# Performance work log

Hardware: AMD Instinct MI355X
Metric: run time of the kernel (lower is better)

The kernel has to match this reference:

```python
import jax, jax.numpy as jnp
import numpy as np
from jax import lax

B, C, H, W = 16, 1, 1024, 1024
BOUNDARY_WEIGHT = 3.0
# two iterations of a flat 5x5 structuring element == one flat 9x9 window
WIN = 9
PAD = WIN // 2


def setup_inputs() -> dict:
    key = jax.random.key(0)
    k1, k2, k3, k4 = jax.random.split(key, 4)
    logits = jax.random.normal(k1, (B, C, H, W), dtype=jnp.float32)
    # spatially-coherent binary masks (random disks), mimicking car masks
    cy = jax.random.uniform(k2, (B,), minval=0.3 * H, maxval=0.7 * H)
    cx = jax.random.uniform(k3, (B,), minval=0.3 * W, maxval=0.7 * W)
    r = jax.random.uniform(k4, (B,), minval=0.15 * H, maxval=0.4 * H)
    ys = jnp.arange(H, dtype=jnp.float32)
    xs = jnp.arange(W, dtype=jnp.float32)
    d2 = (ys[None, :, None] - cy[:, None, None]) ** 2 + (xs[None, None, :] - cx[:, None, None]) ** 2
    targets = (d2 < (r[:, None, None] ** 2)).astype(jnp.float32)[:, None]  # [B,1,H,W]
    return {"logits": logits, "targets": targets}


def _morph(t, op, init):
    # flat-SE morphology over HxW via reduce_window; cv2 default border is
    # the neutral value for the op, matching init padding.
    return lax.reduce_window(
        t, init, op,
        window_dimensions=(1, 1, WIN, WIN),
        window_strides=(1, 1, 1, 1),
        padding=[(0, 0), (0, 0), (PAD, PAD), (PAD, PAD)],
    )


def reference(logits, targets):
    dilated = _morph(targets, lax.max, -jnp.inf)
    eroded = _morph(targets, lax.min, jnp.inf)
    boundary = dilated - eroded  # 1 on mask boundary band, else 0
    weights = 1.0 + (BOUNDARY_WEIGHT - 1.0) * boundary
    # stable BCE-with-logits: max(x,0) - x*y + log1p(exp(-|x|))
    x, y = logits, targets
    per_elem = jnp.maximum(x, 0.0) - x * y + jax.nn.softplus(-jnp.abs(x))
    return jnp.mean(weights * per_elem)
```

## Files before the change

kernel.cpp:

```cpp
#include <hip/hip_runtime.h>

#define BATCH 16
#define IMG_H 1024
#define IMG_W 1024
#define WORDS 16
#define TOTAL_WORDS (BATCH * IMG_H * WORDS)
typedef unsigned long long u64;

#define PK_NT 256
#define PK_BLOCKS 8192
#define PK_WAVES (PK_NT / 64)
#define GROUPS (TOTAL_WORDS / 4)
#define PK_ITERS (GROUPS / (PK_BLOCKS * PK_WAVES))

__global__ __launch_bounds__(PK_NT, 8)
void wbce_pack_kernel(const float* __restrict__ tgt, u64* __restrict__ pak)
{
    const int lane = threadIdx.x & 63;
    const int gw   = blockIdx.x * PK_WAVES + (threadIdx.x >> 6);
    #pragma unroll
    for (int i = 0; i < PK_ITERS; ++i) {
        int g = gw + i * (PK_BLOCKS * PK_WAVES);
        const float* p = tgt + (size_t)g * 256 + lane;
        float v0 = p[0], v1 = p[64], v2 = p[128], v3 = p[192];
        u64 m0 = __ballot(v0 > 0.5f);
        u64 m1 = __ballot(v1 > 0.5f);
        u64 m2 = __ballot(v2 > 0.5f);
        u64 m3 = __ballot(v3 > 0.5f);
        if (lane == 0) {
            ulonglong2* q = (ulonglong2*)(pak + (size_t)g * 4);
            q[0] = make_ulonglong2(m0, m1);
            q[1] = make_ulonglong2(m2, m3);
        }
    }
}

#define MO_NT 256
__global__ __launch_bounds__(MO_NT, 8)
void wbce_morph_kernel(const u64* __restrict__ pak, uint4* __restrict__ tbnd)
{
    const int idx = blockIdx.x * MO_NT + threadIdx.x;
    const int w   = idx & 15;
    const int row = (idx >> 4) & (IMG_H - 1);
    const int img = idx >> 14;
    const u64* ib = pak + (size_t)img * (IMG_H * WORDS);

    u64 d = 0ULL, e = ~0ULL, C = 0ULL;
    const int r0 = row >= 4 ? row - 4 : 0;
    const int r1 = row <= IMG_H - 5 ? row + 4 : IMG_H - 1;
    for (int r = r0; r <= r1; ++r) {
        const u64* rp = ib + (size_t)r * WORDS;
        u64 c  = rp[w];
        u64 P  = (w > 0)  ? rp[w - 1] : 0ULL;
        u64 N  = (w < 15) ? rp[w + 1] : 0ULL;
        u64 Pe = (w > 0)  ? P : ~0ULL;
        u64 Ne = (w < 15) ? N : ~0ULL;
        u64 hd = c, he = c;
        #pragma unroll
        for (int s = 1; s <= 4; ++s) {
            hd |= (c >> s) | (N  << (64 - s));
            hd |= (c << s) | (P  >> (64 - s));
            he &= (c >> s) | (Ne << (64 - s));
            he &= (c << s) | (Pe >> (64 - s));
        }
        d |= hd;
        e &= he;
        if (r == row) C = c;
    }
    u64 bnd = d & ~e;
    tbnd[idx] = make_uint4((unsigned)C,          (unsigned)bnd,
                           (unsigned)(C >> 32),  (unsigned)(bnd >> 32));
}

#define BC_NT 256
#define BC_THREADS (BATCH * IMG_H * IMG_W / 8)
#define BC_BLOCKS (BC_THREADS / BC_NT)
#define BC_NWAVES (BC_NT / 64)

__device__ __forceinline__ float bce4(float4 x4, unsigned tw, unsigned bw, int sh)
{
    float acc = 0.0f;
    const float xs[4] = {x4.x, x4.y, x4.z, x4.w};
    #pragma unroll
    for (int j = 0; j < 4; ++j) {
        unsigned tbit = (tw >> (sh + j)) & 1u;
        unsigned bbit = (bw >> (sh + j)) & 1u;
        unsigned xu   = __float_as_uint(xs[j]);
        float sgn = __uint_as_float(xu ^ (tbit << 31));
        float a   = __uint_as_float(xu & 0x7fffffffu);
        float t   = __builtin_exp2f(a * -1.44269504088896340736f);
        float l2  = __builtin_log2f(1.0f + t);
        float pe  = fmaf(l2, 0.69314718055994530942f, fmaxf(sgn, 0.0f));
        float wg  = fmaf((float)bbit, 2.0f, 1.0f);
        acc = fmaf(wg, pe, acc);
    }
    return acc;
}

__global__ __launch_bounds__(BC_NT, 8)
void wbce_bce_kernel(const float* __restrict__ logits,
                     const uint2* __restrict__ tbnd,
                     float* __restrict__ partial)
{
    __shared__ float sRed[BC_NWAVES];
    const int tid = threadIdx.x;
    const int t   = blockIdx.x * BC_NT + tid;
    const float4* lg4 = (const float4*)logits;

    float4 f0 = lg4[t];
    float4 f1 = lg4[t + BC_THREADS];
    uint2 tb0 = tbnd[t >> 3];
    uint2 tb1 = tbnd[(t >> 3) + (BC_THREADS >> 3)];
    const int sh = (t & 7) * 4;

    float acc = bce4(f0, tb0.x, tb0.y, sh) + bce4(f1, tb1.x, tb1.y, sh);

    #pragma unroll
    for (int off = 32; off > 0; off >>= 1)
        acc += __shfl_down(acc, off, 64);
    const int lane = tid & 63, wv = tid >> 6;
    if (lane == 0) sRed[wv] = acc;
    __syncthreads();
    if (tid == 0) {
        float s = 0.0f;
        #pragma unroll
        for (int i = 0; i < BC_NWAVES; ++i) s += sRed[i];
        partial[blockIdx.x] = s;
    }
}

#define FR_NT 1024
__global__ __launch_bounds__(FR_NT, 1)
void wbce_final_kernel(const float* __restrict__ partial, float* __restrict__ out)
{
    __shared__ float sRed[FR_NT / 64];
    const int tid = threadIdx.x;
    const float4* p4 = (const float4*)partial;
    float4 a = p4[tid];
    float4 b = p4[tid + FR_NT];
    float acc = (a.x + a.y) + (a.z + a.w) + (b.x + b.y) + (b.z + b.w);
    #pragma unroll
    for (int off = 32; off > 0; off >>= 1)
        acc += __shfl_down(acc, off, 64);
    if ((tid & 63) == 0) sRed[tid >> 6] = acc;
    __syncthreads();
    if (tid == 0) {
        float s = 0.0f;
        #pragma unroll
        for (int i = 0; i < FR_NT / 64; ++i) s += sRed[i];
        out[0] = s * (1.0f / 16777216.0f);
    }
}

extern "C" void kernel_launch(void* const* d_in, const int* in_sizes, int n_in,
                              void* d_out, int out_size, void* d_ws, size_t ws_size,
                              hipStream_t stream) {
    const float* logits  = (const float*)d_in[0];
    const float* targets = (const float*)d_in[1];
    float* out = (float*)d_out;

    u64*   pak     = (u64*)d_ws;
    uint4* tbnd    = (uint4*)((char*)d_ws + (2u << 20));
    float* partial = (float*)((char*)d_ws + (6u << 20));

    wbce_pack_kernel<<<dim3(PK_BLOCKS), dim3(PK_NT), 0, stream>>>(targets, pak);

    wbce_morph_kernel<<<dim3(TOTAL_WORDS / MO_NT), dim3(MO_NT), 0, stream>>>(pak, tbnd);

    wbce_bce_kernel<<<dim3(BC_BLOCKS), dim3(BC_NT), 0, stream>>>(
        logits, (const uint2*)tbnd, partial);

    wbce_final_kernel<<<dim3(1), dim3(FR_NT), 0, stream>>>(partial, out);
}
```

Baseline: 42.31 us.

## Fuse target packing with unweighted BCE; add sparse boundary correction pass

The first kernel now reads logits and targets together, packs the target bits and accumulates the unweighted BCE in a single pass. The morphology kernel then compacts the words that contain boundary pixels into a list via an atomic counter. A third kernel revisits only those words and adds the extra boundary-weighted term, re-reading only the boundary logits. This is meant to remove a full second read of the logits, at the cost of atomics, a compacted list, and an extra kernel whose work depends on the input.

```diff
diff --git a/kernel.cpp b/kernel.cpp
--- a/kernel.cpp
+++ b/kernel.cpp
@@ -4,48 +4,90 @@
 #define IMG_H 1024
 #define IMG_W 1024
 #define WORDS 16
-#define TOTAL_WORDS (BATCH * IMG_H * WORDS)
+#define TOTAL_PX (BATCH * IMG_H * IMG_W)
+#define TOTAL_WORDS (TOTAL_PX / 64)
 typedef unsigned long long u64;
 
-#define PK_NT 256
-#define PK_BLOCKS 8192
-#define PK_WAVES (PK_NT / 64)
-#define GROUPS (TOTAL_WORDS / 4)
-#define PK_ITERS (GROUPS / (PK_BLOCKS * PK_WAVES))
-
-__global__ __launch_bounds__(PK_NT, 8)
-void wbce_pack_kernel(const float* __restrict__ tgt, u64* __restrict__ pak)
-{
-    const int lane = threadIdx.x & 63;
-    const int gw   = blockIdx.x * PK_WAVES + (threadIdx.x >> 6);
-    #pragma unroll
-    for (int i = 0; i < PK_ITERS; ++i) {
-        int g = gw + i * (PK_BLOCKS * PK_WAVES);
-        const float* p = tgt + (size_t)g * 256 + lane;
-        float v0 = p[0], v1 = p[64], v2 = p[128], v3 = p[192];
-        u64 m0 = __ballot(v0 > 0.5f);
-        u64 m1 = __ballot(v1 > 0.5f);
-        u64 m2 = __ballot(v2 > 0.5f);
-        u64 m3 = __ballot(v3 > 0.5f);
-        if (lane == 0) {
-            ulonglong2* q = (ulonglong2*)(pak + (size_t)g * 4);
-            q[0] = make_ulonglong2(m0, m1);
-            q[1] = make_ulonglong2(m2, m3);
-        }
-    }
-}
-
-#define MO_NT 256
-__global__ __launch_bounds__(MO_NT, 8)
-void wbce_morph_kernel(const u64* __restrict__ pak, uint4* __restrict__ tbnd)
-{
-    const int idx = blockIdx.x * MO_NT + threadIdx.x;
+__device__ __forceinline__ float bce1(float x, bool y)
+{
+    unsigned xu = __float_as_uint(x);
+    float sgn = __uint_as_float(xu ^ (y ? 0x80000000u : 0u));
+    float a   = __uint_as_float(xu & 0x7fffffffu);
+    float t   = __builtin_exp2f(a * -1.44269504088896340736f);
+    float l2  = __builtin_log2f(1.0f + t);
+    return fmaf(l2, 0.69314718055994530942f, fmaxf(sgn, 0.0f));
+}
+
+#define A_NT 256
+#define A_WPB (A_NT / 64)
+#define A_BLOCKS (TOTAL_WORDS / 8 / A_WPB)
+
+__global__ __launch_bounds__(A_NT, 8)
+void wbce_main_kernel(const float* __restrict__ logits,
+                      const float* __restrict__ targets,
+                      u64* __restrict__ pak,
+                      unsigned* __restrict__ cnt,
+                      float* __restrict__ partial)
+{
+    __shared__ float sRed[A_WPB];
+    const int tid  = threadIdx.x;
+    const int lane = tid & 63;
+    const int wv   = tid >> 6;
+    if (blockIdx.x == 0 && tid == 0) cnt[0] = 0;
+
+    const int gw = blockIdx.x * A_WPB + wv;
+    const size_t base = (size_t)gw * 512 + lane;
+    const float* tp = targets + base;
+    const float* lp = logits  + base;
+
+    float tv[8], lv[8];
+    #pragma unroll
+    for (int j = 0; j < 8; ++j) tv[j] = tp[64 * j];
+    #pragma unroll
+    for (int j = 0; j < 8; ++j) lv[j] = lp[64 * j];
+
+    u64 bm[8];
+    #pragma unroll
+    for (int j = 0; j < 8; ++j) bm[j] = __ballot(tv[j] > 0.5f);
+    if (lane == 0) {
+        ulonglong2* q = (ulonglong2*)(pak + (size_t)gw * 8);
+        q[0] = make_ulonglong2(bm[0], bm[1]);
+        q[1] = make_ulonglong2(bm[2], bm[3]);
+        q[2] = make_ulonglong2(bm[4], bm[5]);
+        q[3] = make_ulonglong2(bm[6], bm[7]);
+    }
+
+    float acc = 0.0f;
+    #pragma unroll
+    for (int j = 0; j < 8; ++j) acc += bce1(lv[j], tv[j] > 0.5f);
+
+    #pragma unroll
+    for (int off = 32; off > 0; off >>= 1)
+        acc += __shfl_down(acc, off, 64);
+    if (lane == 0) sRed[wv] = acc;
+    __syncthreads();
+    if (tid == 0) {
+        float s = 0.0f;
+        #pragma unroll
+        for (int i = 0; i < A_WPB; ++i) s += sRed[i];
+        partial[blockIdx.x] = s;
+    }
+}
+
+#define B_NT 256
+__global__ __launch_bounds__(B_NT, 8)
+void wbce_morph_kernel(const u64* __restrict__ pak,
+                       u64* __restrict__ bndArr,
+                       unsigned* __restrict__ list,
+                       unsigned* __restrict__ cnt)
+{
+    const int idx = blockIdx.x * B_NT + threadIdx.x;
     const int w   = idx & 15;
     const int row = (idx >> 4) & (IMG_H - 1);
     const int img = idx >> 14;
     const u64* ib = pak + (size_t)img * (IMG_H * WORDS);
 
-    u64 d = 0ULL, e = ~0ULL, C = 0ULL;
+    u64 d = 0ULL, e = ~0ULL;
     const int r0 = row >= 4 ? row - 4 : 0;
     const int r1 = row <= IMG_H - 5 ? row + 4 : IMG_H - 1;
     for (int r = r0; r <= r1; ++r) {
@@ -65,80 +107,80 @@
         }
         d |= hd;
         e &= he;
-        if (r == row) C = c;
     }
     u64 bnd = d & ~e;
-    tbnd[idx] = make_uint4((unsigned)C,          (unsigned)bnd,
-                           (unsigned)(C >> 32),  (unsigned)(bnd >> 32));
-}
-
-#define BC_NT 256
-#define BC_THREADS (BATCH * IMG_H * IMG_W / 8)
-#define BC_BLOCKS (BC_THREADS / BC_NT)
-#define BC_NWAVES (BC_NT / 64)
-
-__device__ __forceinline__ float bce4(float4 x4, unsigned tw, unsigned bw, int sh)
-{
+    bndArr[idx] = bnd;
+
+    const int lane = threadIdx.x & 63;
+    u64 mask = __ballot(bnd != 0ULL);
+    int nb = __popcll(mask);
+    unsigned base = 0;
+    if (lane == 0 && nb) base = atomicAdd(cnt, (unsigned)nb);
+    base = (unsigned)__shfl((int)base, 0, 64);
+    if (bnd != 0ULL) {
+        int off = __popcll(mask & ((1ULL << lane) - 1ULL));
+        list[base + off] = (unsigned)idx;
+    }
+}
+
+#define C_NT 256
+#define C_BLOCKS 2048
+#define C_WAVES (C_BLOCKS * (C_NT / 64))
+
+__global__ __launch_bounds__(C_NT, 8)
+void wbce_bnd_kernel(const float* __restrict__ logits,
+                     const u64* __restrict__ pak,
+                     const u64* __restrict__ bndArr,
+                     const unsigned* __restrict__ list,
+                     const unsigned* __restrict__ cnt,
+                     float* __restrict__ partial2)
+{
+    __shared__ float sRed[C_NT / 64];
+    const int tid = threadIdx.x, lane = tid & 63, wv = tid >> 6;
+    const int gw  = blockIdx.x * (C_NT / 64) + wv;
+    const unsigned n = cnt[0];
+
     float acc = 0.0f;
-    const float xs[4] = {x4.x, x4.y, x4.z, x4.w};
-    #pragma unroll
-    for (int j = 0; j < 4; ++j) {
-        unsigned tbit = (tw >> (sh + j)) & 1u;
-        unsigned bbit = (bw >> (sh + j)) & 1u;
-        unsigned xu   = __float_as_uint(xs[j]);
-        float sgn = __uint_as_float(xu ^ (tbit << 31));
-        float a   = __uint_as_float(xu & 0x7fffffffu);
-        float t   = __builtin_exp2f(a * -1.44269504088896340736f);
-        float l2  = __builtin_log2f(1.0f + t);
-        float pe  = fmaf(l2, 0.69314718055994530942f, fmaxf(sgn, 0.0f));
-        float wg  = fmaf((float)bbit, 2.0f, 1.0f);
-        acc = fmaf(wg, pe, acc);
-    }
-    return acc;
-}
-
-__global__ __launch_bounds__(BC_NT, 8)
-void wbce_bce_kernel(const float* __restrict__ logits,
-                     const uint2* __restrict__ tbnd,
-                     float* __restrict__ partial)
-{
-    __shared__ float sRed[BC_NWAVES];
-    const int tid = threadIdx.x;
-    const int t   = blockIdx.x * BC_NT + tid;
-    const float4* lg4 = (const float4*)logits;
-
-    float4 f0 = lg4[t];
-    float4 f1 = lg4[t + BC_THREADS];
-    uint2 tb0 = tbnd[t >> 3];
-    uint2 tb1 = tbnd[(t >> 3) + (BC_THREADS >> 3)];
-    const int sh = (t & 7) * 4;
-
-    float acc = bce4(f0, tb0.x, tb0.y, sh) + bce4(f1, tb1.x, tb1.y, sh);
+    for (unsigned e = gw; e < n; e += C_WAVES) {
+        unsigned idx = list[e];
+        u64 bnd = bndArr[idx];
+        u64 Cw  = pak[idx];
+        bool act = (bnd >> lane) & 1ULL;
+        float x = 0.0f;
+        if (act) x = logits[((size_t)idx << 6) + lane];
+        float pe = bce1(x, ((Cw >> lane) & 1ULL) != 0ULL);
+        acc += act ? 2.0f * pe : 0.0f;
+    }
 
     #pragma unroll
     for (int off = 32; off > 0; off >>= 1)
         acc += __shfl_down(acc, off, 64);
-    const int lane = tid & 63, wv = tid >> 6;
     if (lane == 0) sRed[wv] = acc;
     __syncthreads();
     if (tid == 0) {
         float s = 0.0f;
         #pragma unroll
-        for (int i = 0; i < BC_NWAVES; ++i) s += sRed[i];
-        partial[blockIdx.x] = s;
-    }
-}
-
-#define FR_NT 1024
-__global__ __launch_bounds__(FR_NT, 1)
-void wbce_final_kernel(const float* __restrict__ partial, float* __restrict__ out)
-{
-    __shared__ float sRed[FR_NT / 64];
+        for (int i = 0; i < C_NT / 64; ++i) s += sRed[i];
+        partial2[blockIdx.x] = s;
+    }
+}
+
+#define D_NT 1024
+__global__ __launch_bounds__(D_NT, 1)
+void wbce_final_kernel(const float* __restrict__ partial,
+                       const float* __restrict__ partial2,
+                       float* __restrict__ out)
+{
+    __shared__ float sRed[D_NT / 64];
     const int tid = threadIdx.x;
     const float4* p4 = (const float4*)partial;
     float4 a = p4[tid];
-    float4 b = p4[tid + FR_NT];
+    float4 b = p4[tid + D_NT];
     float acc = (a.x + a.y) + (a.z + a.w) + (b.x + b.y) + (b.z + b.w);
+    if (tid < 512) {
+        float4 c = ((const float4*)partial2)[tid];
+        acc += (c.x + c.y) + (c.z + c.w);
+    }
     #pragma unroll
     for (int off = 32; off > 0; off >>= 1)
         acc += __shfl_down(acc, off, 64);
@@ -147,7 +189,7 @@
     if (tid == 0) {
         float s = 0.0f;
         #pragma unroll
-        for (int i = 0; i < FR_NT / 64; ++i) s += sRed[i];
+        for (int i = 0; i < D_NT / 64; ++i) s += sRed[i];
         out[0] = s * (1.0f / 16777216.0f);
     }
 }
@@ -159,16 +201,22 @@
     const float* targets = (const float*)d_in[1];
     float* out = (float*)d_out;
 
-    u64*   pak     = (u64*)d_ws;
-    uint4* tbnd    = (uint4*)((char*)d_ws + (2u << 20));
-    float* partial = (float*)((char*)d_ws + (6u << 20));
-
-    wbce_pack_kernel<<<dim3(PK_BLOCKS), dim3(PK_NT), 0, stream>>>(targets, pak);
-
-    wbce_morph_kernel<<<dim3(TOTAL_WORDS / MO_NT), dim3(MO_NT), 0, stream>>>(pak, tbnd);
-
-    wbce_bce_kernel<<<dim3(BC_BLOCKS), dim3(BC_NT), 0, stream>>>(
-        logits, (const uint2*)tbnd, partial);
-
-    wbce_final_kernel<<<dim3(1), dim3(FR_NT), 0, stream>>>(partial, out);
-}
+    char* ws = (char*)d_ws;
+    u64*      pak      = (u64*)ws;
+    u64*      bndArr   = (u64*)(ws + (2u << 20));
+    unsigned* list     = (unsigned*)(ws + (4u << 20));
+    unsigned* cnt      = (unsigned*)(ws + (5u << 20));
+    float*    partial  = (float*)(ws + (5u << 20) + 4096);
+    float*    partial2 = (float*)(ws + (5u << 20) + 4096 + 32768);
+
+    wbce_main_kernel<<<dim3(A_BLOCKS), dim3(A_NT), 0, stream>>>(
+        logits, targets, pak, cnt, partial);
+
+    wbce_morph_kernel<<<dim3(TOTAL_WORDS / B_NT), dim3(B_NT), 0, stream>>>(
+        pak, bndArr, list, cnt);
+
+    wbce_bnd_kernel<<<dim3(C_BLOCKS), dim3(C_NT), 0, stream>>>(
+        logits, pak, bndArr, list, cnt, partial2);
+
+    wbce_final_kernel<<<dim3(1), dim3(D_NT), 0, stream>>>(partial, partial2, out);
+}
```

Result: slower. 65.79 us (+55.5%).

## Stream logits into LDS via global_load_lds with split waitcnt pipelining in BCE kernel

Applied to the files above, without the earlier changes.

The BCE kernel now has each 256-thread block cover 8192 logits. It loads them with direct global-to-LDS DMA (global_load_lds, 16 bytes per lane) and issues eight mask-word loads through inline assembly. It waits on only the first half of the loads before computing, so the second half overlaps the work. The final reduction shrinks to 512 threads to match the smaller partial count. The trade-off is fewer, larger blocks with 32KB of LDS each, which lowers occupancy. The hand-written waitcnt/barrier ordering is fragile: a wave's vmcnt wait covers only its own loads, and the s_barrier is what makes the other waves' LDS writes visible.

```diff
diff --git a/kernel.cpp b/kernel.cpp
--- a/kernel.cpp
+++ b/kernel.cpp
@@ -4,8 +4,28 @@
 #define IMG_H 1024
 #define IMG_W 1024
 #define WORDS 16
-#define TOTAL_WORDS (BATCH * IMG_H * WORDS)
+#define TOTAL_PX (BATCH * IMG_H * IMG_W)
+#define TOTAL_WORDS (TOTAL_PX / 64)
 typedef unsigned long long u64;
+typedef unsigned u32x2 __attribute__((ext_vector_type(2)));
+
+__device__ __forceinline__ float bce1(float x, bool y)
+{
+    unsigned xu = __float_as_uint(x);
+    float sgn = __uint_as_float(xu ^ (y ? 0x80000000u : 0u));
+    float a   = __uint_as_float(xu & 0x7fffffffu);
+    float t   = __builtin_exp2f(a * -1.44269504088896340736f);
+    float l2  = __builtin_log2f(1.0f + t);
+    return fmaf(l2, 0.69314718055994530942f, fmaxf(sgn, 0.0f));
+}
+
+__device__ __forceinline__ void g2l16(const float* g, float* l)
+{
+    __builtin_amdgcn_global_load_lds(
+        (const __attribute__((address_space(1))) void*)g,
+        (__attribute__((address_space(3))) void*)l,
+        16, 0, 0);
+}
 
 #define PK_NT 256
 #define PK_BLOCKS 8192
@@ -68,77 +88,108 @@
         if (r == row) C = c;
     }
     u64 bnd = d & ~e;
-    tbnd[idx] = make_uint4((unsigned)C,          (unsigned)bnd,
-                           (unsigned)(C >> 32),  (unsigned)(bnd >> 32));
+    tbnd[idx] = make_uint4((unsigned)C,         (unsigned)bnd,
+                           (unsigned)(C >> 32), (unsigned)(bnd >> 32));
 }
 
 #define BC_NT 256
-#define BC_THREADS (BATCH * IMG_H * IMG_W / 8)
-#define BC_BLOCKS (BC_THREADS / BC_NT)
-#define BC_NWAVES (BC_NT / 64)
-
-__device__ __forceinline__ float bce4(float4 x4, unsigned tw, unsigned bw, int sh)
-{
+#define BC_FLOATS 8192
+#define BC_BLOCKS (TOTAL_PX / BC_FLOATS)
+
+__global__ __launch_bounds__(BC_NT, 4)
+void wbce_bce_kernel(const float* __restrict__ logits,
+                     const uint2* __restrict__ tbnd2,
+                     float* __restrict__ partial)
+{
+    __shared__ float sX[BC_FLOATS];
+    __shared__ float sRed[BC_NT / 64];
+    const int tid = threadIdx.x, lane = tid & 63, wv = tid >> 6;
+    const size_t blockFloat = (size_t)blockIdx.x * BC_FLOATS;
+
+    const uint2* ta = tbnd2 + (size_t)blockIdx.x * 256 + (tid >> 3);
+    u32x2 tb0, tb1, tb2, tb3, tb4, tb5, tb6, tb7;
+    asm volatile(
+        "global_load_dwordx2 %0, %8, off\n\t"
+        "global_load_dwordx2 %1, %8, off offset:256\n\t"
+        "global_load_dwordx2 %2, %8, off offset:512\n\t"
+        "global_load_dwordx2 %3, %8, off offset:768\n\t"
+        "global_load_dwordx2 %4, %8, off offset:1024\n\t"
+        "global_load_dwordx2 %5, %8, off offset:1280\n\t"
+        "global_load_dwordx2 %6, %8, off offset:1536\n\t"
+        "global_load_dwordx2 %7, %8, off offset:1792"
+        : "=&v"(tb0), "=&v"(tb1), "=&v"(tb2), "=&v"(tb3),
+          "=&v"(tb4), "=&v"(tb5), "=&v"(tb6), "=&v"(tb7)
+        : "v"(ta));
+
+    #pragma unroll
+    for (int j = 0; j < 4; ++j)
+        g2l16(logits + blockFloat + wv * 1024 + j * 256 + lane * 4,
+              sX + wv * 1024 + j * 256);
+    #pragma unroll
+    for (int j = 0; j < 4; ++j)
+        g2l16(logits + blockFloat + 4096 + wv * 1024 + j * 256 + lane * 4,
+              sX + 4096 + wv * 1024 + j * 256);
+
+    asm volatile("s_waitcnt vmcnt(4)"
+        : "+v"(tb0), "+v"(tb1), "+v"(tb2), "+v"(tb3) :: "memory");
+    __builtin_amdgcn_sched_barrier(0);
+    __builtin_amdgcn_s_barrier();
+
+    const float4* sX4 = (const float4*)sX;
+    const int sh = (tid & 7) * 4;
     float acc = 0.0f;
-    const float xs[4] = {x4.x, x4.y, x4.z, x4.w};
-    #pragma unroll
-    for (int j = 0; j < 4; ++j) {
-        unsigned tbit = (tw >> (sh + j)) & 1u;
-        unsigned bbit = (bw >> (sh + j)) & 1u;
-        unsigned xu   = __float_as_uint(xs[j]);
-        float sgn = __uint_as_float(xu ^ (tbit << 31));
-        float a   = __uint_as_float(xu & 0x7fffffffu);
-        float t   = __builtin_exp2f(a * -1.44269504088896340736f);
-        float l2  = __builtin_log2f(1.0f + t);
-        float pe  = fmaf(l2, 0.69314718055994530942f, fmaxf(sgn, 0.0f));
-        float wg  = fmaf((float)bbit, 2.0f, 1.0f);
-        acc = fmaf(wg, pe, acc);
-    }
-    return acc;
-}
-
-__global__ __launch_bounds__(BC_NT, 8)
-void wbce_bce_kernel(const float* __restrict__ logits,
-                     const uint2* __restrict__ tbnd,
-                     float* __restrict__ partial)
-{
-    __shared__ float sRed[BC_NWAVES];
-    const int tid = threadIdx.x;
-    const int t   = blockIdx.x * BC_NT + tid;
-    const float4* lg4 = (const float4*)logits;
-
-    float4 f0 = lg4[t];
-    float4 f1 = lg4[t + BC_THREADS];
-    uint2 tb0 = tbnd[t >> 3];
-    uint2 tb1 = tbnd[(t >> 3) + (BC_THREADS >> 3)];
-    const int sh = (t & 7) * 4;
-
-    float acc = bce4(f0, tb0.x, tb0.y, sh) + bce4(f1, tb1.x, tb1.y, sh);
+
+    #define CONSUME(k, tb)                                                    \
+    do {                                                                      \
+        float4 x4 = sX4[(k) * 256 + tid];                                     \
+        unsigned tw = (tb).x, bw = (tb).y;                                    \
+        const float xs[4] = {x4.x, x4.y, x4.z, x4.w};                         \
+        _Pragma("unroll")                                                     \
+        for (int j = 0; j < 4; ++j) {                                         \
+            unsigned tbit = (tw >> (sh + j)) & 1u;                            \
+            unsigned bbit = (bw >> (sh + j)) & 1u;                            \
+            unsigned xu   = __float_as_uint(xs[j]);                           \
+            float sgn = __uint_as_float(xu ^ (tbit << 31));                   \
+            float av  = __uint_as_float(xu & 0x7fffffffu);                    \
+            float t   = __builtin_exp2f(av * -1.44269504088896340736f);       \
+            float l2  = __builtin_log2f(1.0f + t);                            \
+            float pe  = fmaf(l2, 0.69314718055994530942f, fmaxf(sgn, 0.0f));  \
+            float wg  = fmaf((float)bbit, 2.0f, 1.0f);  \
+            acc = fmaf(wg, pe, acc);                                          \
+        }                                                                     \
+    } while (0)
+
+    CONSUME(0, tb0); CONSUME(1, tb1); CONSUME(2, tb2); CONSUME(3, tb3);
+
+    asm volatile("s_waitcnt vmcnt(0)"
+        : "+v"(tb4), "+v"(tb5), "+v"(tb6), "+v"(tb7) :: "memory");
+    __builtin_amdgcn_sched_barrier(0);
+    __builtin_amdgcn_s_barrier();
+
+    CONSUME(4, tb4); CONSUME(5, tb5); CONSUME(6, tb6); CONSUME(7, tb7);
+    #undef CONSUME
 
     #pragma unroll
     for (int off = 32; off > 0; off >>= 1)
         acc += __shfl_down(acc, off, 64);
-    const int lane = tid & 63, wv = tid >> 6;
     if (lane == 0) sRed[wv] = acc;
     __syncthreads();
     if (tid == 0) {
         float s = 0.0f;
         #pragma unroll
-        for (int i = 0; i < BC_NWAVES; ++i) s += sRed[i];
+        for (int i = 0; i < BC_NT / 64; ++i) s += sRed[i];
         partial[blockIdx.x] = s;
     }
 }
 
-#define FR_NT 1024
+#define FR_NT 512
 __global__ __launch_bounds__(FR_NT, 1)
 void wbce_final_kernel(const float* __restrict__ partial, float* __restrict__ out)
 {
     __shared__ float sRed[FR_NT / 64];
     const int tid = threadIdx.x;
-    const float4* p4 = (const float4*)partial;
-    float4 a = p4[tid];
-    float4 b = p4[tid + FR_NT];
-    float acc = (a.x + a.y) + (a.z + a.w) + (b.x + b.y) + (b.z + b.w);
+    float4 a = ((const float4*)partial)[tid];
+    float acc = (a.x + a.y) + (a.z + a.w);
     #pragma unroll
     for (int off = 32; off > 0; off >>= 1)
         acc += __shfl_down(acc, off, 64);
@@ -159,9 +210,10 @@
     const float* targets = (const float*)d_in[1];
     float* out = (float*)d_out;
 
-    u64*   pak     = (u64*)d_ws;
-    uint4* tbnd    = (uint4*)((char*)d_ws + (2u << 20));
-    float* partial = (float*)((char*)d_ws + (6u << 20));
+    char* ws = (char*)d_ws;
+    u64*   pak     = (u64*)ws;
+    uint4* tbnd    = (uint4*)(ws + (2u << 20));
+    float* partial = (float*)(ws + (6u << 20));
 
     wbce_pack_kernel<<<dim3(PK_BLOCKS), dim3(PK_NT), 0, stream>>>(targets, pak);
 
```

Result: slower. 44.15 us (+4.3%).
